# Optimization experiments

Measured on AMD Instinct MI355X. Metric: run time of the kernel, lower is better.

The kernel has to match this reference:

```python
import jax, jax.numpy as jnp
import numpy as np
from jax import lax

LEAK = 0.2
EPS = 1e-5
T = 20  # sequence_length


def _lrelu(x):
    return jnp.where(x >= 0, x, LEAK * x)


def _deconv(x, w, stride=2, k=4, p=1):
    # PyTorch ConvTranspose2d(weight [in,out,kH,kW], stride=2, pad=1) equivalent:
    # flip kernel spatially, swap in/out channels, use lhs_dilation.
    wt = jnp.flip(w, (2, 3)).transpose(1, 0, 2, 3)  # OIHW
    pad = k - 1 - p
    return lax.conv_general_dilated(
        x, wt, window_strides=(1, 1), padding=[(pad, pad), (pad, pad)],
        lhs_dilation=(stride, stride),
        dimension_numbers=('NCHW', 'OIHW', 'NCHW'))


def _bn(x, g, b):
    # BatchNorm2d, training mode (batch statistics, biased variance)
    m = x.mean((0, 2, 3), keepdims=True)
    v = x.var((0, 2, 3), keepdims=True)
    return (x - m) * lax.rsqrt(v + EPS) * g[None, :, None, None] + b[None, :, None, None]


def setup_inputs() -> dict:
    B, CD, MD, H, FF = 64, 128, 128, 256, 512
    ks = jax.random.split(jax.random.key(0), 32)
    rn = lambda k, sh, s=0.02: (s * jax.random.normal(k, sh)).astype(jnp.float32)
    return {
        'z_content': jax.random.normal(ks[0], (B, CD), jnp.float32),
        'z_motion': jax.random.normal(ks[1], (B, MD), jnp.float32),
        'W_h': rn(ks[2], (H, CD + MD)), 'b_h': jnp.zeros((H,), jnp.float32),
        'W_c': rn(ks[3], (H, CD + MD)), 'b_c': jnp.zeros((H,), jnp.float32),
        'W_ih': rn(ks[4], (4 * H, H)), 'W_hh': rn(ks[5], (4 * H, H)),
        'b_ih': jnp.zeros((4 * H,), jnp.float32), 'b_hh': jnp.zeros((4 * H,), jnp.float32),
        'W_f': rn(ks[6], (FF, H)), 'b_f': jnp.zeros((FF,), jnp.float32),
        'init_in': rn(ks[7], (1, H), 0.1),
        'fc_W': rn(ks[8], (256 * 4 * 4, FF + CD)), 'fc_b': jnp.zeros((256 * 16,), jnp.float32),
        'w0': rn(ks[9], (256, 128, 4, 4)), 'g0': jnp.ones((128,), jnp.float32), 'be0': jnp.zeros((128,), jnp.float32),
        'w1': rn(ks[10], (128, 64, 4, 4)), 'g1': jnp.ones((64,), jnp.float32), 'be1': jnp.zeros((64,), jnp.float32),
        'w2': rn(ks[11], (64, 32, 4, 4)), 'g2': jnp.ones((32,), jnp.float32), 'be2': jnp.zeros((32,), jnp.float32),
        'wf': rn(ks[12], (32, 1, 4, 4)), 'bf': jnp.zeros((1,), jnp.float32),
    }


def reference(z_content, z_motion, W_h, b_h, W_c, b_c, W_ih, W_hh, b_ih, b_hh,
              W_f, b_f, init_in, fc_W, fc_b, w0, g0, be0, w1, g1, be1,
              w2, g2, be2, wf, bf):
    B = z_content.shape[0]
    z = jnp.concatenate([z_content, z_motion], axis=-1)
    h0 = z @ W_h.T + b_h  # [B,H]
    c0 = z @ W_c.T + b_c
    x0 = jnp.broadcast_to(init_in, (B, init_in.shape[1]))
    bias = b_ih + b_hh

    def step(carry, _):
        x, h, c = carry
        gates = x @ W_ih.T + h @ W_hh.T + bias  # [B,4H], torch gate order i,f,g,o
        i, f, g, o = jnp.split(gates, 4, axis=-1)
        c_new = jax.nn.sigmoid(f) * c + jax.nn.sigmoid(i) * jnp.tanh(g)
        h_new = jax.nn.sigmoid(o) * jnp.tanh(c_new)
        return (h_new, h_new, c_new), h_new

    _, outs = lax.scan(step, (x0, h0, c0), None, length=T)  # [T,B,H]
    outs = outs.transpose(1, 0, 2)  # [B,T,H]

    ff = _lrelu(outs @ W_f.T + b_f)  # [B,T,FF]
    zc = jnp.broadcast_to(z_content[:, None, :], (B, T, z_content.shape[1]))
    feat = jnp.concatenate([ff, zc], axis=-1).reshape(B * T, -1)  # [B*T, FF+CD]

    h = _lrelu(feat @ fc_W.T + fc_b).reshape(B * T, 256, 4, 4)
    h = _lrelu(_bn(_deconv(h, w0), g0, be0))   # [B*T,128,8,8]
    h = _lrelu(_bn(_deconv(h, w1), g1, be1))   # [B*T,64,16,16]
    h = _lrelu(_bn(_deconv(h, w2), g2, be2))   # [B*T,32,32,32]
    out = jax.nn.sigmoid(_deconv(h, wf) + bf[None, :, None, None])  # [B*T,1,64,64]
    return out.reshape(B, T, *out.shape[1:])
```

## Files before the change

kernel.cpp:

```cpp
#include <hip/hip_runtime.h>
#include <hip/hip_bf16.h>
#include <math.h>

typedef __hip_bfloat16 bf16;
typedef __attribute__((ext_vector_type(8))) short bf16x8;
typedef __attribute__((ext_vector_type(4))) float f32x4;
typedef __attribute__((ext_vector_type(2))) float f32x2;

#define LRELU(v) ((v) > 0.f ? (v) : 0.2f*(v))

__device__ __forceinline__ float sig_f(float x){ return 1.f/(1.f + __expf(-x)); }
__device__ __forceinline__ float tanh_f(float x){
  float ax = fabsf(x);
  float e = __expf(-2.f*ax);
  float t = (1.f - e)/(1.f + e);
  return x >= 0.f ? t : -t;
}
__device__ __forceinline__ ushort bfbits(float v){
  bf16 b = __float2bfloat16(v);
  return *(ushort*)&b;
}
__device__ __forceinline__ uint bfpack(float a, float b){
  return (uint)bfbits(a) | ((uint)bfbits(b) << 16);
}
__device__ __forceinline__ float bflo(uint u){ return __uint_as_float(u << 16); }
__device__ __forceinline__ float bfhi(uint u){ return __uint_as_float(u & 0xffff0000u); }

template<int CI, int CO>
__device__ __forceinline__ void wprep_body(const float* __restrict__ w,
                                           ushort* __restrict__ wpn, int e){
  constexpr int K = 4*CI, KF = K/32, MMW2 = CO/16;
  if (e >= 16*CI*CO) return;
  int j  = e & 7;
  int lk = (e >> 3) & 3;
  int lm = (e >> 5) & 15;
  int r3 = e >> 9;
  int kf = r3 % KF; int r4 = r3 / KF;
  int m  = r4 % MMW2; int p = r4 / MMW2;
  int k  = kf*32 + lk*8 + j;
  int t  = k / CI, ci = k % CI;
  int co = m*16 + lm;
  int py = p >> 1, px = p & 1, dy = t >> 1, dx = t & 1;
  int ky = (py ? 0 : 1) + 2*dy;
  int kx = (px ? 0 : 1) + 2*dx;
  wpn[e] = bfbits(w[((ci*CO + co)*4 + ky)*4 + kx]);
}

__global__ __launch_bounds__(256) void k_prep(
    const float* __restrict__ W_h, const float* __restrict__ W_c,
    float* __restrict__ WhT, float* __restrict__ WcT,
    const float* __restrict__ fc_W, ushort* __restrict__ wpfc,
    const float* __restrict__ W_f, ushort* __restrict__ wpff,
    const float* __restrict__ Wih, const float* __restrict__ Whh,
    uint4* __restrict__ Whq8, uint4* __restrict__ Wsq8, float* __restrict__ stats,
    const float* __restrict__ b_ih, const float* __restrict__ b_hh,
    const float* __restrict__ init_in,
    float4* __restrict__ xg4, float4* __restrict__ bias4,
    const float* __restrict__ w0, ushort* __restrict__ wp0,
    const float* __restrict__ w1, ushort* __restrict__ wp1,
    const float* __restrict__ w2, ushort* __restrict__ wp2,
    const float* __restrict__ wf, ushort* __restrict__ wfb)
{
  __shared__ float t[32][33];
  __shared__ float4 red[4];
  const int b = blockIdx.x, tid = threadIdx.x;

  if (b < 128) {
    const float* src = (b < 64) ? W_h : W_c;
    float* dst = (b < 64) ? WhT : WcT;
    int bb = b & 63;
    int c0 = (bb & 7)*32, r0 = (bb >> 3)*32;
    int tx = tid & 31, ty = tid >> 5;
    #pragma unroll
    for (int i = 0; i < 4; ++i)
      t[ty+8*i][tx] = src[(size_t)(r0+ty+8*i)*256 + c0+tx];
    __syncthreads();
    #pragma unroll
    for (int i = 0; i < 4; ++i)
      dst[(size_t)(c0+ty+8*i)*256 + r0+tx] = t[tx][ty+8*i];
    return;
  }
  if (b < 10368) {
    int i = (b - 128)*256 + tid;
    if (i < 2621440) wpfc[i] = bfbits(fc_W[i]);
    return;
  }
  if (b < 10880) {
    int i = (b - 10368)*256 + tid;
    if (i < 131072) wpff[i] = bfbits(W_f[i]);
    return;
  }
  if (b < 10944) {
    int k4 = b - 10880, j = tid;
    if (k4 < 2) { int i = k4*256 + j; if (i < 448) stats[i] = 0.f; }
    uint h4[4], s4[4];
    #pragma unroll
    for (int d = 0; d < 4; ++d) {
      int k = 4*k4 + d;
      float hi = Whh[j*256+k],       hf = Whh[(256+j)*256+k];
      float hg = Whh[(512+j)*256+k], ho = Whh[(768+j)*256+k];
      float ii = Wih[j*256+k],       iff = Wih[(256+j)*256+k];
      float ig = Wih[(512+j)*256+k], io = Wih[(768+j)*256+k];
      int lo = __builtin_amdgcn_cvt_pk_fp8_f32(hi, hf, 0, false);
      h4[d] = (uint)__builtin_amdgcn_cvt_pk_fp8_f32(hg, ho, lo, true);
      lo = __builtin_amdgcn_cvt_pk_fp8_f32(hi+ii, hf+iff, 0, false);
      s4[d] = (uint)__builtin_amdgcn_cvt_pk_fp8_f32(hg+ig, ho+io, lo, true);
    }
    Whq8[k4*256+j] = make_uint4(h4[0], h4[1], h4[2], h4[3]);
    Wsq8[k4*256+j] = make_uint4(s4[0], s4[1], s4[2], s4[3]);
    return;
  }
  if (b < 11200) {
    int bb = b - 10944, tt = tid;
    float v = init_in[tt];
    float p0 = v * Wih[bb*256 + tt];
    float p1 = v * Wih[(256+bb)*256 + tt];
    float p2 = v * Wih[(512+bb)*256 + tt];
    float p3 = v * Wih[(768+bb)*256 + tt];
    #pragma unroll
    for (int o = 32; o; o >>= 1) {
      p0 += __shfl_xor(p0, o); p1 += __shfl_xor(p1, o);
      p2 += __shfl_xor(p2, o); p3 += __shfl_xor(p3, o);
    }
    int lane = tt & 63, wid = tt >> 6;
    if (lane == 0) red[wid] = make_float4(p0,p1,p2,p3);
    __syncthreads();
    if (tt == 0) {
      float4 bi = make_float4(b_ih[bb]+b_hh[bb], b_ih[256+bb]+b_hh[256+bb],
                              b_ih[512+bb]+b_hh[512+bb], b_ih[768+bb]+b_hh[768+bb]);
      bias4[bb] = bi;
      float4 a = bi;
      #pragma unroll
      for (int w = 0; w < 4; ++w) { a.x += red[w].x; a.y += red[w].y; a.z += red[w].z; a.w += red[w].w; }
      xg4[bb] = a;
    }
    return;
  }
  if (b < 13248) { wprep_body<256,128>(w0, wp0, (b - 11200)*256 + tid); return; }
  if (b < 13760) { wprep_body<128,64>(w1, wp1, (b - 13248)*256 + tid); return; }
  if (b < 13888) { wprep_body<64,32>(w2, wp2, (b - 13760)*256 + tid); return; }
  {
    int e = (b - 13888)*256 + tid;
    if (e < 512) {
      int tt = e >> 5, ci = e & 31;
      wfb[tt*32 + ci] = bfbits(wf[ci*16 + tt]);
    }
  }
}

__global__ __launch_bounds__(256) void k_h0c0(const float* __restrict__ zc, const float* __restrict__ zm,
                      const float* __restrict__ WhT, const float* __restrict__ WcT,
                      const float* __restrict__ b_h, const float* __restrict__ b_c,
                      float* __restrict__ h, float* __restrict__ c){
  __shared__ float zs[256];
  int b = blockIdx.x, j = threadIdx.x;
  zs[j] = (j < 128) ? zc[b*128 + j] : zm[b*128 + (j-128)];
  __syncthreads();
  float ah = b_h[j], ac = b_c[j];
  #pragma unroll 4
  for (int k = 0; k < 256; ++k) {
    float zv = zs[k];
    ah = fmaf(zv, WhT[k*256 + j], ah);
    ac = fmaf(zv, WcT[k*256 + j], ac);
  }
  h[b*256+j] = ah; c[b*256+j] = ac;
}

__global__ __launch_bounds__(1024) void k_lstm_all(
    const uint4* __restrict__ Whq8, const uint4* __restrict__ Wsq8,
    const float4* __restrict__ xg4, const float4* __restrict__ bias4,
    const float* __restrict__ h0, const float* __restrict__ c0,
    ushort* __restrict__ outsb){
  __shared__ float hs[256];
  __shared__ float4 part[3][256];
  const int b = blockIdx.x, tid = threadIdx.x;
  const int j = tid & 255, kq = tid >> 8;
  float cj = 0.f;
  if (kq == 0) { hs[j] = h0[b*256 + j]; cj = c0[b*256 + j]; }
  __syncthreads();
  for (int t = 0; t < 20; ++t) {
    const uint4* __restrict__ Wp = ((t == 0) ? Whq8 : Wsq8) + (size_t)(kq*16)*256 + j;
    float4 a = make_float4(0.f, 0.f, 0.f, 0.f);
    #pragma unroll 8
    for (int kk = 0; kk < 16; ++kk) {
      uint4 wv = Wp[(size_t)kk*256];
      const float* __restrict__ hb = &hs[kq*64 + 4*kk];
      {
        f32x2 pif = __builtin_amdgcn_cvt_pk_f32_fp8((int)wv.x, false);
        f32x2 pgo = __builtin_amdgcn_cvt_pk_f32_fp8((int)wv.x, true);
        float hv = hb[0];
        a.x = fmaf(hv, pif[0], a.x); a.y = fmaf(hv, pif[1], a.y);
        a.z = fmaf(hv, pgo[0], a.z); a.w = fmaf(hv, pgo[1], a.w);
      }
      {
        f32x2 pif = __builtin_amdgcn_cvt_pk_f32_fp8((int)wv.y, false);
        f32x2 pgo = __builtin_amdgcn_cvt_pk_f32_fp8((int)wv.y, true);
        float hv = hb[1];
        a.x = fmaf(hv, pif[0], a.x); a.y = fmaf(hv, pif[1], a.y);
        a.z = fmaf(hv, pgo[0], a.z); a.w = fmaf(hv, pgo[1], a.w);
      }
      {
        f32x2 pif = __builtin_amdgcn_cvt_pk_f32_fp8((int)wv.z, false);
        f32x2 pgo = __builtin_amdgcn_cvt_pk_f32_fp8((int)wv.z, true);
        float hv = hb[2];
        a.x = fmaf(hv, pif[0], a.x); a.y = fmaf(hv, pif[1], a.y);
        a.z = fmaf(hv, pgo[0], a.z); a.w = fmaf(hv, pgo[1], a.w);
      }
      {
        f32x2 pif = __builtin_amdgcn_cvt_pk_f32_fp8((int)wv.w, false);
        f32x2 pgo = __builtin_amdgcn_cvt_pk_f32_fp8((int)wv.w, true);
        float hv = hb[3];
        a.x = fmaf(hv, pif[0], a.x); a.y = fmaf(hv, pif[1], a.y);
        a.z = fmaf(hv, pgo[0], a.z); a.w = fmaf(hv, pgo[1], a.w);
      }
    }
    if (kq) part[kq-1][j] = a;
    __syncthreads();
    if (kq == 0) {
      float4 p1 = part[0][j], p2 = part[1][j], p3 = part[2][j];
      float4 bb = (t == 0) ? xg4[j] : bias4[j];
      a.x += p1.x + p2.x + p3.x + bb.x;
      a.y += p1.y + p2.y + p3.y + bb.y;
      a.z += p1.z + p2.z + p3.z + bb.z;
      a.w += p1.w + p2.w + p3.w + bb.w;
      float ig = sig_f(a.x), fg = sig_f(a.y), gg = tanh_f(a.z), og = sig_f(a.w);
      cj = fmaf(fg, cj, ig*gg);
      float hj = og * tanh_f(cj);
      outsb[(b*20 + t)*256 + j] = bfbits(hj);
      hs[j] = hj;
    }
    __syncthreads();
  }
}

__global__ __launch_bounds__(256) void k_ff_m(
    const ushort* __restrict__ A, const ushort* __restrict__ W,
    const float* __restrict__ bias, const float* __restrict__ zc,
    ushort* __restrict__ C)
{
  constexpr int K = 256, BK = 64, NK = K/BK, BM = 128, BN = 64;
  constexpr int RS = 72;
  constexpr int NCF = BN/16;
  constexpr int AC = 4, WC = 2;

  __shared__ __align__(16) ushort Al[2][BM*RS];
  __shared__ __align__(16) ushort Wl[2][BN*RS];

  const int tid = threadIdx.x;
  const int col0 = blockIdx.x * BN, row0 = blockIdx.y * BM;
  const int w = tid >> 6, l = tid & 63, lm = l & 15, lk = l >> 4;

  f32x4 acc[NCF][2];
  #pragma unroll
  for (int m = 0; m < NCF; ++m)
    #pragma unroll
    for (int s = 0; s < 2; ++s)
      acc[m][s] = (f32x4){0.f,0.f,0.f,0.f};

  uint4 ar[AC], wr[WC];

  #define LOADG(kt) { \
    _Pragma("unroll") \
    for (int i = 0; i < AC; ++i) { \
      int chunk = tid + i*256; \
      int rl = chunk >> 3, kc = chunk & 7; \
      ar[i] = *(const uint4*)&A[(size_t)(row0+rl)*K + (kt)*BK + kc*8]; \
    } \
    _Pragma("unroll") \
    for (int i = 0; i < WC; ++i) { \
      int chunk = tid + i*256; \
      int co = chunk >> 3, kc = chunk & 7; \
      wr[i] = *(const uint4*)&W[(size_t)(col0+co)*K + (kt)*BK + kc*8]; \
    } }

  #define STOREL(buf) { \
    _Pragma("unroll") \
    for (int i = 0; i < AC; ++i) { \
      int chunk = tid + i*256; \
      int rl = chunk >> 3, kc = chunk & 7; \
      *(uint4*)&Al[buf][rl*RS + kc*8] = ar[i]; \
    } \
    _Pragma("unroll") \
    for (int i = 0; i < WC; ++i) { \
      int chunk = tid + i*256; \
      int co = chunk >> 3, kc = chunk & 7; \
      *(uint4*)&Wl[buf][co*RS + kc*8] = wr[i]; \
    } }

  LOADG(0);
  STOREL(0);
  int cur = 0;
  for (int kt = 0; kt < NK; ++kt) {
    if (kt + 1 < NK) LOADG(kt + 1);
    __syncthreads();
    #pragma unroll
    for (int kf = 0; kf < 2; ++kf) {
      bf16x8 bfr[2];
      #pragma unroll
      for (int s = 0; s < 2; ++s)
        bfr[s] = *(bf16x8*)&Al[cur][(w*32 + s*16 + lm)*RS + kf*32 + lk*8];
      #pragma unroll
      for (int m = 0; m < NCF; ++m) {
        bf16x8 afr = *(bf16x8*)&Wl[cur][(m*16 + lm)*RS + kf*32 + lk*8];
        acc[m][0] = __builtin_amdgcn_mfma_f32_16x16x32_bf16(afr, bfr[0], acc[m][0], 0, 0, 0);
        acc[m][1] = __builtin_amdgcn_mfma_f32_16x16x32_bf16(afr, bfr[1], acc[m][1], 0, 0, 0);
      }
    }
    if (kt + 1 < NK) STOREL(cur ^ 1);
    cur ^= 1;
  }

  #pragma unroll
  for (int m = 0; m < NCF; ++m) {
    #pragma unroll
    for (int s = 0; s < 2; ++s) {
      int row = row0 + w*32 + s*16 + lm;
      f32x4 v = acc[m][s];
      int u0 = col0 + m*16 + lk*4;
      union { ushort u[4]; uint2 q; } pk;
      #pragma unroll
      for (int j = 0; j < 4; ++j)
        pk.u[j] = bfbits(LRELU(v[j] + bias[u0+j]));
      *(uint2*)&C[(size_t)row*640 + u0] = pk.q;
    }
  }
  {
    int base = ((int)blockIdx.y*8 + (int)blockIdx.x)*2048 + tid;
    #pragma unroll
    for (int i = 0; i < 8; ++i) {
      int e = base + i*256;
      int r = e >> 7, c2 = e & 127;
      C[r*640 + 512 + c2] = bfbits(zc[(r/20)*128 + c2]);
    }
  }
  #undef LOADG
  #undef STOREL
}

__global__ __launch_bounds__(256) void k_gemm_fc_m(
    const ushort* __restrict__ A, const ushort* __restrict__ W,
    const float* __restrict__ bias, ushort* __restrict__ C)
{
  constexpr int K = 640, BK = 64, NK = K/BK, BM = 128, BN = 64;
  constexpr int RS = 72;
  constexpr int NCF = BN/16;
  constexpr int AC = 4, WC = 2;

  __shared__ __align__(16) ushort Al[2][BM*RS];
  __shared__ __align__(16) ushort Wl[2][BN*RS];

  const int tid = threadIdx.x;
  const int col0 = blockIdx.x * BN, row0 = blockIdx.y * BM;
  const int w = tid >> 6, l = tid & 63, lm = l & 15, lk = l >> 4;

  f32x4 acc[NCF][2];
  #pragma unroll
  for (int m = 0; m < NCF; ++m)
    #pragma unroll
    for (int s = 0; s < 2; ++s)
      acc[m][s] = (f32x4){0.f,0.f,0.f,0.f};

  uint4 ar[AC], wr[WC];

  #define LOADG(kt) { \
    _Pragma("unroll") \
    for (int i = 0; i < AC; ++i) { \
      int chunk = tid + i*256; \
      int rl = chunk >> 3, kc = chunk & 7; \
      ar[i] = *(const uint4*)&A[(size_t)(row0+rl)*K + (kt)*BK + kc*8]; \
    } \
    _Pragma("unroll") \
    for (int i = 0; i < WC; ++i) { \
      int chunk = tid + i*256; \
      int co = chunk >> 3, kc = chunk & 7; \
      wr[i] = *(const uint4*)&W[(size_t)(col0+co)*K + (kt)*BK + kc*8]; \
    } }

  #define STOREL(buf) { \
    _Pragma("unroll") \
    for (int i = 0; i < AC; ++i) { \
      int chunk = tid + i*256; \
      int rl = chunk >> 3, kc = chunk & 7; \
      *(uint4*)&Al[buf][rl*RS + kc*8] = ar[i]; \
    } \
    _Pragma("unroll") \
    for (int i = 0; i < WC; ++i) { \
      int chunk = tid + i*256; \
      int co = chunk >> 3, kc = chunk & 7; \
      *(uint4*)&Wl[buf][co*RS + kc*8] = wr[i]; \
    } }

  LOADG(0);
  STOREL(0);
  int cur = 0;
  for (int kt = 0; kt < NK; ++kt) {
    if (kt + 1 < NK) LOADG(kt + 1);
    __syncthreads();
    #pragma unroll
    for (int kf = 0; kf < 2; ++kf) {
      bf16x8 bfr[2];
      #pragma unroll
      for (int s = 0; s < 2; ++s)
        bfr[s] = *(bf16x8*)&Al[cur][(w*32 + s*16 + lm)*RS + kf*32 + lk*8];
      #pragma unroll
      for (int m = 0; m < NCF; ++m) {
        bf16x8 afr = *(bf16x8*)&Wl[cur][(m*16 + lm)*RS + kf*32 + lk*8];
        acc[m][0] = __builtin_amdgcn_mfma_f32_16x16x32_bf16(afr, bfr[0], acc[m][0], 0, 0, 0);
        acc[m][1] = __builtin_amdgcn_mfma_f32_16x16x32_bf16(afr, bfr[1], acc[m][1], 0, 0, 0);
      }
    }
    if (kt + 1 < NK) STOREL(cur ^ 1);
    cur ^= 1;
  }

  #pragma unroll
  for (int m = 0; m < NCF; ++m) {
    #pragma unroll
    for (int s = 0; s < 2; ++s) {
      int row = row0 + w*32 + s*16 + lm;
      f32x4 v = acc[m][s];
      #pragma unroll
      for (int j = 0; j < 4; ++j) {
        int u = col0 + m*16 + lk*4 + j;
        float val = LRELU(v[j] + bias[u]);
        C[((size_t)row << 12) + ((size_t)(u & 15) << 8) + (u >> 4)] = bfbits(val);
      }
    }
  }
  #undef LOADG
  #undef STOREL
}

template<int CI, int CO, int HI>
__global__ __attribute__((amdgpu_flat_work_group_size(256, 256), amdgpu_waves_per_eu(2, 4)))
void k_dcv(
    const ushort* __restrict__ in, const ushort* __restrict__ wp,
    ushort* __restrict__ out, float* __restrict__ gsum, float* __restrict__ gsq)
{
  constexpr int WI = HI, HO = 2*HI, WO = 2*WI;
  constexpr int K = 4*CI, KFT = K/32;
  constexpr int BSP = 128;
  constexpr int NCF = CO/32;
  constexpr int COH = CO/2;

  __shared__ float s_sum[COH], s_sq[COH];

  const int tid = threadIdx.x;
  const int sp0 = blockIdx.x * BSP;
  const int p  = blockIdx.y;
  const int coz = blockIdx.z;
  const int py = p >> 1, px = p & 1;
  const int w  = tid >> 6, l = tid & 63;
  const int lm = l & 15, lk = l >> 4;

  if (tid < COH) { s_sum[tid] = 0.f; s_sq[tid] = 0.f; }

  f32x4 acc[NCF][2];
  #pragma unroll
  for (int m = 0; m < NCF; ++m)
    #pragma unroll
    for (int s = 0; s < 2; ++s)
      acc[m][s] = (f32x4){0.f,0.f,0.f,0.f};

  int pn[2], poy[2], pox[2];
  #pragma unroll
  for (int s = 0; s < 2; ++s) {
    int sp = sp0 + w*32 + s*16 + lm;
    pn[s] = sp / (HI*WI);
    int rem = sp % (HI*WI);
    poy[s] = rem / WI; pox[s] = rem % WI;
  }

  const ushort* wpb = wp + (size_t)(p*(CO/16) + coz*NCF)*KFT*512;

  bf16x8 afrN[NCF];
  #pragma unroll
  for (int m = 0; m < NCF; ++m)
    afrN[m] = *(const bf16x8*)&wpb[((size_t)m*KFT)*512 + lm*32 + lk*8];

  for (int ktg = 0; ktg < KFT; ++ktg) {
    const int t = (ktg*32)/CI;
    const int ci0 = (ktg*32)%CI + lk*8;
    const int dy = t >> 1, dx = t & 1;
    bf16x8 afr[NCF];
    #pragma unroll
    for (int m = 0; m < NCF; ++m) afr[m] = afrN[m];
    if (ktg + 1 < KFT) {
      #pragma unroll
      for (int m = 0; m < NCF; ++m)
        afrN[m] = *(const bf16x8*)&wpb[((size_t)m*KFT + ktg + 1)*512 + lm*32 + lk*8];
    }
    bf16x8 bfr[2];
    #pragma unroll
    for (int s = 0; s < 2; ++s) {
      int iy = poy[s] + py - dy, ix = pox[s] + px - dx;
      bool valid = ((unsigned)iy < (unsigned)HI) && ((unsigned)ix < (unsigned)WI);
      if (valid)
        bfr[s] = *(const bf16x8*)&in[((((size_t)pn[s]*HI + iy)*WI + ix)*CI) + ci0];
      else
        bfr[s] = (bf16x8){0,0,0,0,0,0,0,0};
    }
    #pragma unroll
    for (int m = 0; m < NCF; ++m) {
      acc[m][0] = __builtin_amdgcn_mfma_f32_16x16x32_bf16(afr[m], bfr[0], acc[m][0], 0, 0, 0);
      acc[m][1] = __builtin_amdgcn_mfma_f32_16x16x32_bf16(afr[m], bfr[1], acc[m][1], 0, 0, 0);
    }
  }

  #pragma unroll
  for (int m = 0; m < NCF; ++m) {
    float s1[4] = {0,0,0,0}, s2[4] = {0,0,0,0};
    #pragma unroll
    for (int s = 0; s < 2; ++s) {
      f32x4 v = acc[m][s];
      #pragma unroll
      for (int j = 0; j < 4; ++j) { s1[j] += v[j]; s2[j] += v[j]*v[j]; }
    }
    #pragma unroll
    for (int j = 0; j < 4; ++j) {
      float a = s1[j], b = s2[j];
      #pragma unroll
      for (int o = 1; o < 16; o <<= 1) { a += __shfl_xor(a, o); b += __shfl_xor(b, o); }
      if (lm == 0) {
        atomicAdd(&s_sum[m*16 + lk*4 + j], a);
        atomicAdd(&s_sq [m*16 + lk*4 + j], b);
      }
    }
  }
  #pragma unroll
  for (int s = 0; s < 2; ++s) {
    int y = 2*poy[s] + py, x = 2*pox[s] + px;
    size_t ob = (((size_t)pn[s]*HO + y)*WO + x)*CO + coz*COH + lk*4;
    #pragma unroll
    for (int m = 0; m < NCF; ++m) {
      f32x4 v = acc[m][s];
      union { ushort u[4]; uint2 q; } pk;
      pk.u[0] = bfbits(v[0]); pk.u[1] = bfbits(v[1]);
      pk.u[2] = bfbits(v[2]); pk.u[3] = bfbits(v[3]);
      *(uint2*)&out[ob + m*16] = pk.q;
    }
  }
  __syncthreads();
  for (int cc = tid; cc < COH; cc += 256) {
    atomicAdd(&gsum[coz*COH + cc], s_sum[cc]);
    atomicAdd(&gsq[coz*COH + cc],  s_sq[cc]);
  }
}

template<int CI, int CO, int HI>
__global__ __attribute__((amdgpu_flat_work_group_size(512, 512), amdgpu_waves_per_eu(2, 4)))
void k_dcvim(
    const ushort* __restrict__ in, const ushort* __restrict__ wp,
    const float* __restrict__ gsumP, const float* __restrict__ gsqP,
    const float* __restrict__ gP, const float* __restrict__ beP, float invNP,
    ushort* __restrict__ out, float* __restrict__ gsum, float* __restrict__ gsq)
{
  constexpr int WI = HI, HO = 2*HI, WO = 2*WI;
  constexpr int K = 4*CI;
  constexpr int KF = K/32;
  constexpr int PAD = HI + 2;
  constexpr int CICH = CI/8;
  constexpr int MMW2 = CO/16;
  constexpr int SFTH = HI*WI/32;

  __shared__ __align__(16) ushort Ain[PAD*PAD*CI];
  __shared__ float s_sum[CO], s_sq[CO];
  __shared__ float s_scale[CI], s_shift[CI];

  const int tid = threadIdx.x;
  const int n = blockIdx.x;
  const int w = tid >> 6, l = tid & 63, lm = l & 15, lk = l >> 4;
  const int p = w >> 1, py = p >> 1, px = p & 1, ph = w & 1;

  if (tid < CO) { s_sum[tid] = 0.f; s_sq[tid] = 0.f; }
  if (tid >= 512-CI) {
    int c = tid - (512-CI);
    float m = gsumP[c]*invNP;
    float v = gsqP[c]*invNP - m*m;
    float sc = gP[c]*rsqrtf(v + 1e-5f);
    s_scale[c] = sc;
    s_shift[c] = beP[c] - m*sc;
  }
  __syncthreads();

  const ushort* inb = in + (size_t)n * HI * WI * CI;
  constexpr int NPCH = PAD*PAD*CICH;
  for (int e = tid; e < NPCH; e += 512) {
    int ci8 = e % CICH; int sp = e / CICH;
    int c = sp % PAD, r = sp / PAD;
    int chS = ci8 ^ (c & 7);
    if (r >= 1 && r <= HI && c >= 1 && c <= WI) {
      uint4 u = *(const uint4*)&inb[(((size_t)(r-1)*WI + (c-1))*CI) + ci8*8];
      int ci0 = ci8*8;
      float4 sc0 = *(const float4*)&s_scale[ci0];
      float4 sc1 = *(const float4*)&s_scale[ci0+4];
      float4 sh0 = *(const float4*)&s_shift[ci0];
      float4 sh1 = *(const float4*)&s_shift[ci0+4];
      float v0 = LRELU(fmaf(bflo(u.x), sc0.x, sh0.x));
      float v1 = LRELU(fmaf(bfhi(u.x), sc0.y, sh0.y));
      float v2 = LRELU(fmaf(bflo(u.y), sc0.z, sh0.z));
      float v3 = LRELU(fmaf(bfhi(u.y), sc0.w, sh0.w));
      float v4 = LRELU(fmaf(bflo(u.z), sc1.x, sh1.x));
      float v5 = LRELU(fmaf(bfhi(u.z), sc1.y, sh1.y));
      float v6 = LRELU(fmaf(bflo(u.w), sc1.z, sh1.z));
      float v7 = LRELU(fmaf(bfhi(u.w), sc1.w, sh1.w));
      uint4 o;
      o.x = (uint)bfpack(v0, v1);
      o.y = (uint)bfpack(v2, v3);
      o.z = (uint)bfpack(v4, v5);
      o.w = (uint)bfpack(v6, v7);
      ((uint4*)Ain)[(r*PAD + c)*CICH + chS] = o;
    } else {
      ((uint4*)Ain)[(r*PAD + c)*CICH + chS] = make_uint4(0,0,0,0);
    }
  }
  __syncthreads();

  f32x4 acc[MMW2][SFTH];
  #pragma unroll
  for (int m = 0; m < MMW2; ++m)
    #pragma unroll
    for (int sf = 0; sf < SFTH; ++sf)
      acc[m][sf] = (f32x4){0.f,0.f,0.f,0.f};

  const ushort* wpb = wp + (size_t)(p*MMW2)*KF*512;
  bf16x8 afrN[MMW2];
  #pragma unroll
  for (int m = 0; m < MMW2; ++m)
    afrN[m] = *(const bf16x8*)&wpb[((size_t)m*KF)*512 + lm*32 + lk*8];
  #pragma unroll
  for (int kf = 0; kf < KF; ++kf) {
    const int t = (kf*32)/CI, cib = (kf*32)%CI;
    const int dy = t >> 1, dx = t & 1;
    bf16x8 afr[MMW2];
    #pragma unroll
    for (int m = 0; m < MMW2; ++m) afr[m] = afrN[m];
    if (kf + 1 < KF) {
      #pragma unroll
      for (int m = 0; m < MMW2; ++m)
        afrN[m] = *(const bf16x8*)&wpb[((size_t)m*KF + (kf+1))*512 + lm*32 + lk*8];
    }
    const int ch = (cib >> 3) + lk;
    #pragma unroll
    for (int sf = 0; sf < SFTH; ++sf) {
      int s = (ph*SFTH + sf)*16 + lm;
      int y = s / WI, x = s % WI;
      int r = y + py - dy + 1, c = x + px - dx + 1;
      bf16x8 bfr = *(const bf16x8*)&Ain[((r*PAD + c)*CICH + (ch ^ (c & 7)))*8];
      #pragma unroll
      for (int m = 0; m < MMW2; ++m)
        acc[m][sf] = __builtin_amdgcn_mfma_f32_16x16x32_bf16(afr[m], bfr, acc[m][sf], 0, 0, 0);
    }
  }

  float s1[MMW2][4], s2[MMW2][4];
  #pragma unroll
  for (int m = 0; m < MMW2; ++m)
    #pragma unroll
    for (int j = 0; j < 4; ++j) { s1[m][j] = 0.f; s2[m][j] = 0.f; }

  #pragma unroll
  for (int sf = 0; sf < SFTH; ++sf) {
    int s = (ph*SFTH + sf)*16 + lm;
    int y = 2*(s / WI) + py, x = 2*(s % WI) + px;
    size_t ob = (((size_t)n*HO + y)*WO + x)*CO + lk*4;
    #pragma unroll
    for (int m = 0; m < MMW2; ++m) {
      f32x4 v = acc[m][sf];
      union { ushort u[4]; uint2 q; } pk;
      #pragma unroll
      for (int j = 0; j < 4; ++j) {
        pk.u[j] = bfbits(v[j]);
        s1[m][j] += v[j];
        s2[m][j] += v[j]*v[j];
      }
      *(uint2*)&out[ob + m*16] = pk.q;
    }
  }

  #pragma unroll
  for (int m = 0; m < MMW2; ++m) {
    #pragma unroll
    for (int j = 0; j < 4; ++j) {
      float a = s1[m][j], b = s2[m][j];
      #pragma unroll
      for (int o = 1; o < 16; o <<= 1) { a += __shfl_xor(a, o); b += __shfl_xor(b, o); }
      if (lm == 0) {
        atomicAdd(&s_sum[m*16 + lk*4 + j], a);
        atomicAdd(&s_sq [m*16 + lk*4 + j], b);
      }
    }
  }

  __syncthreads();
  for (int cc = tid; cc < CO; cc += 512) {
    atomicAdd(&gsum[cc], s_sum[cc]);
    atomicAdd(&gsq[cc],  s_sq[cc]);
  }
}

__global__ __launch_bounds__(256) void k_final(
    const ushort* __restrict__ in, const ushort* __restrict__ wfb,
    const float* __restrict__ gsumP, const float* __restrict__ gsqP,
    const float* __restrict__ gP, const float* __restrict__ beP, float invNP,
    const float* __restrict__ bfb, float* __restrict__ outp)
{
  constexpr int CI=32, HI=32, WI=32, HO=64, WO=64, SPLIT=4, HOq=HO/SPLIT;
  constexpr int RMAX = 10;
  constexpr int DP = 20;
  __shared__ float Dl[RMAX*32*DP];
  __shared__ float s_scale[CI], s_shift[CI];

  const int tid = threadIdx.x, bid = blockIdx.x;
  const int n = bid % 1280, q = bid / 1280;
  const int y0 = q * HOq;
  const int rows_lo = max(0, y0/2 - 1);
  const int rows_hi = min(HI-1, (y0 + HOq)/2);
  const int nrows = rows_hi - rows_lo + 1;

  if (tid < CI) {
    float m = gsumP[tid]*invNP;
    float v = gsqP[tid]*invNP - m*m;
    float sc = gP[tid]*rsqrtf(v + 1e-5f);
    s_scale[tid] = sc;
    s_shift[tid] = beP[tid] - m*sc;
  }
  __syncthreads();

  const int w = tid >> 6, l = tid & 63, lm = l & 15, lk = l >> 4;
  const bf16x8 afr = *(const bf16x8*)&wfb[lm*32 + lk*8];
  const float4 sc0 = *(const float4*)&s_scale[lk*8];
  const float4 sc1 = *(const float4*)&s_scale[lk*8+4];
  const float4 sh0 = *(const float4*)&s_shift[lk*8];
  const float4 sh1 = *(const float4*)&s_shift[lk*8+4];

  const ushort* inb = in + (size_t)n * HI * WI * CI;
  const int ngrp = nrows * 2;
  for (int g = w; g < ngrp; g += 4) {
    int px = g*16 + lm;
    int rl = px >> 5, ix = px & 31;
    uint4 u = *(const uint4*)&inb[(((size_t)(rows_lo+rl)*WI + ix)*CI) + lk*8];
    float v0 = LRELU(fmaf(bflo(u.x), sc0.x, sh0.x));
    float v1 = LRELU(fmaf(bfhi(u.x), sc0.y, sh0.y));
    float v2 = LRELU(fmaf(bflo(u.y), sc0.z, sh0.z));
    float v3 = LRELU(fmaf(bfhi(u.y), sc0.w, sh0.w));
    float v4 = LRELU(fmaf(bflo(u.z), sc1.x, sh1.x));
    float v5 = LRELU(fmaf(bfhi(u.z), sc1.y, sh1.y));
    float v6 = LRELU(fmaf(bflo(u.w), sc1.z, sh1.z));
    float v7 = LRELU(fmaf(bfhi(u.w), sc1.w, sh1.w));
    union { uint uu[4]; bf16x8 v; } pk;
    pk.uu[0] = bfpack(v0, v1);
    pk.uu[1] = bfpack(v2, v3);
    pk.uu[2] = bfpack(v4, v5);
    pk.uu[3] = bfpack(v6, v7);
    f32x4 d = __builtin_amdgcn_mfma_f32_16x16x32_bf16(afr, pk.v, (f32x4){0.f,0.f,0.f,0.f}, 0, 0, 0);
    *(f32x4*)&Dl[px*DP + lk*4] = d;
  }
  __syncthreads();

  const float b0 = bfb[0];
  #pragma unroll
  for (int i = 0; i < (HOq*WO)/256; ++i) {
    int e = tid + i*256;
    int oy = e >> 6, x = e & 63;
    int y = y0 + oy;
    int kya = (y + 1) & 1, iya = (y + 1) >> 1;
    int kxa = (x + 1) & 1, ixa = (x + 1) >> 1;
    float acc = b0;
    #pragma unroll
    for (int dy = 0; dy < 2; ++dy) {
      int iy = iya - dy, ky = kya + 2*dy;
      if (iy < 0 || iy >= HI) continue;
      #pragma unroll
      for (int dx = 0; dx < 2; ++dx) {
        int ix = ixa - dx, kx = kxa + 2*dx;
        if (ix < 0 || ix >= WI) continue;
        acc += Dl[((iy - rows_lo)*WI + ix)*DP + (ky*4 + kx)];
      }
    }
    outp[(size_t)n*HO*WO + y*WO + x] = 1.f/(1.f + __expf(-acc));
  }
}

extern "C" void kernel_launch(void* const* d_in, const int* in_sizes, int n_in,
                              void* d_out, int out_size, void* d_ws, size_t ws_size,
                              hipStream_t stream) {
  const float* z_content = (const float*)d_in[0];
  const float* z_motion  = (const float*)d_in[1];
  const float* W_h  = (const float*)d_in[2];
  const float* b_h  = (const float*)d_in[3];
  const float* W_c  = (const float*)d_in[4];
  const float* b_c  = (const float*)d_in[5];
  const float* W_ih = (const float*)d_in[6];
  const float* W_hh = (const float*)d_in[7];
  const float* b_ih = (const float*)d_in[8];
  const float* b_hh = (const float*)d_in[9];
  const float* W_f  = (const float*)d_in[10];
  const float* b_f  = (const float*)d_in[11];
  const float* init_in = (const float*)d_in[12];
  const float* fc_W = (const float*)d_in[13];
  const float* fc_b = (const float*)d_in[14];
  const float* w0 = (const float*)d_in[15];
  const float* g0 = (const float*)d_in[16];
  const float* be0 = (const float*)d_in[17];
  const float* w1 = (const float*)d_in[18];
  const float* g1 = (const float*)d_in[19];
  const float* be1 = (const float*)d_in[20];
  const float* w2 = (const float*)d_in[21];
  const float* g2 = (const float*)d_in[22];
  const float* be2 = (const float*)d_in[23];
  const float* wf = (const float*)d_in[24];
  const float* bf_ = (const float*)d_in[25];

  const size_t P_BYTES = 10631168;
  const size_t X_OFF   = P_BYTES;
  const size_t X_BYTES = 83886080;
  const size_t Y_OFF   = X_OFF + X_BYTES;
  const size_t NEED    = Y_OFF + 41943040;
  if (ws_size < NEED) return;

  float* ws = (float*)d_ws;
  char*  wsb = (char*)d_ws;
  float* sum0 = ws + 0;        float* sq0 = ws + 128;
  float* sum1 = ws + 256;      float* sq1 = ws + 320;
  float* sum2 = ws + 384;      float* sq2 = ws + 416;
  float4* xg4   = (float4*)(ws + 1024);
  float4* bias4 = (float4*)(ws + 2048);
  float* h    = ws + 3072;
  float* c    = ws + 19456;
  ushort* outsb = (ushort*)(ws + 35840);
  float* WhT  = ws + 199680;
  float* WcT  = ws + 265216;
  uint4* Whq8 = (uint4*)(ws + 330752);
  uint4* Wsq8 = (uint4*)(ws + 592896);
  ushort* wp0 = (ushort*)(ws + 855040);
  ushort* wp1 = (ushort*)(ws + 1117184);
  ushort* wp2 = (ushort*)(ws + 1182720);
  ushort* wfb = (ushort*)(ws + 1199104);
  ushort* wpff = (ushort*)(ws + 1199616);
  ushort* featb = (ushort*)(ws + 1265152);

  ushort* wpfc = (ushort*)(wsb + X_OFF);
  ushort* out0 = (ushort*)(wsb + X_OFF);
  ushort* out2 = (ushort*)(wsb + X_OFF);
  ushort* h1   = (ushort*)(wsb + Y_OFF);
  ushort* out1 = (ushort*)(wsb + Y_OFF);

  k_prep<<<13890, 256, 0, stream>>>(
      W_h, W_c, WhT, WcT, fc_W, wpfc, W_f, wpff,
      W_ih, W_hh, Whq8, Wsq8, ws, b_ih, b_hh, init_in, xg4, bias4,
      w0, wp0, w1, wp1, w2, wp2, wf, wfb);
  k_h0c0<<<64, 256, 0, stream>>>(z_content, z_motion, WhT, WcT, b_h, b_c, h, c);

  k_lstm_all<<<64, 1024, 0, stream>>>(Whq8, Wsq8, xg4, bias4, h, c, outsb);

  k_ff_m<<<dim3(8, 10), 256, 0, stream>>>(outsb, wpff, b_f, z_content, featb);
  k_gemm_fc_m<<<dim3(64, 10), 256, 0, stream>>>(featb, wpfc, fc_b, h1);

  k_dcv<256,128,4><<<dim3(160,4,2), 256, 0, stream>>>(h1, wp0, out0, sum0, sq0);
  k_dcvim<128,64,8><<<1280, 512, 0, stream>>>(out0, wp1, sum0, sq0, g0, be0, 1.f/81920.f, out1, sum1, sq1);
  k_dcvim<64,32,16><<<1280, 512, 0, stream>>>(out1, wp2, sum1, sq1, g1, be1, 1.f/327680.f, out2, sum2, sq2);
  k_final<<<5120, 256, 0, stream>>>(out2, wfb, sum2, sq2, g2, be2, 1.f/1310720.f, bf_, (float*)d_out);
}
```

Baseline: 414.2 us.

## Stage first deconv input images in swizzled LDS, one image per wave

The first transposed-conv layer (4x4 -> 8x8) now loads four whole input images per block into shared memory with an XOR swizzle. Each wave then computes one image's 16 output positions for its parity, reading B fragments from LDS instead of doing bounds-checked global loads. The K loop is fully unrolled and the grid doubles to 320 blocks along x, since each block now covers 64 positions instead of 128. In exchange, each wave issues half as many MFMAs per A-fragment load, which lowers weight reuse, and the kernel needs 32KB of LDS per block.

```diff
diff --git a/kernel.cpp b/kernel.cpp
--- a/kernel.cpp
+++ b/kernel.cpp
@@ -433,44 +433,43 @@
 
 template<int CI, int CO, int HI>
 __global__ __attribute__((amdgpu_flat_work_group_size(256, 256), amdgpu_waves_per_eu(2, 4)))
-void k_dcv(
+void k_dcv0(
     const ushort* __restrict__ in, const ushort* __restrict__ wp,
     ushort* __restrict__ out, float* __restrict__ gsum, float* __restrict__ gsq)
 {
   constexpr int WI = HI, HO = 2*HI, WO = 2*WI;
-  constexpr int K = 4*CI, KFT = K/32;
-  constexpr int BSP = 128;
+  constexpr int KFT = 4*CI/32;
   constexpr int NCF = CO/32;
   constexpr int COH = CO/2;
-
+  constexpr int CICH = CI/8;
+
+  __shared__ __align__(16) ushort Ain[4*16*CI];
   __shared__ float s_sum[COH], s_sq[COH];
 
   const int tid = threadIdx.x;
-  const int sp0 = blockIdx.x * BSP;
-  const int p  = blockIdx.y;
+  const int n0 = blockIdx.x * 4;
+  const int p = blockIdx.y, py = p >> 1, pxp = p & 1;
   const int coz = blockIdx.z;
-  const int py = p >> 1, px = p & 1;
-  const int w  = tid >> 6, l = tid & 63;
-  const int lm = l & 15, lk = l >> 4;
+  const int w = tid >> 6, l = tid & 63, lm = l & 15, lk = l >> 4;
 
   if (tid < COH) { s_sum[tid] = 0.f; s_sq[tid] = 0.f; }
 
-  f32x4 acc[NCF][2];
-  #pragma unroll
-  for (int m = 0; m < NCF; ++m)
-    #pragma unroll
-    for (int s = 0; s < 2; ++s)
-      acc[m][s] = (f32x4){0.f,0.f,0.f,0.f};
-
-  int pn[2], poy[2], pox[2];
-  #pragma unroll
-  for (int s = 0; s < 2; ++s) {
-    int sp = sp0 + w*32 + s*16 + lm;
-    pn[s] = sp / (HI*WI);
-    int rem = sp % (HI*WI);
-    poy[s] = rem / WI; pox[s] = rem % WI;
-  }
-
+  const ushort* inb = in + (size_t)n0 * 16 * CI;
+  #pragma unroll
+  for (int i = 0; i < 8; ++i) {
+    int e = tid + i*256;
+    int ci8 = e & 31; int sp = e >> 5;
+    uint4 u = *(const uint4*)&inb[(size_t)sp*CI + ci8*8];
+    int px = sp & 15;
+    ((uint4*)Ain)[sp*CICH + (ci8 ^ (px & 7))] = u;
+  }
+  __syncthreads();
+
+  f32x4 acc[NCF];
+  #pragma unroll
+  for (int m = 0; m < NCF; ++m) acc[m] = (f32x4){0.f,0.f,0.f,0.f};
+
+  const int oy = lm >> 2, ox = lm & 3;
   const ushort* wpb = wp + (size_t)(p*(CO/16) + coz*NCF)*KFT*512;
 
   bf16x8 afrN[NCF];
@@ -478,47 +477,35 @@
   for (int m = 0; m < NCF; ++m)
     afrN[m] = *(const bf16x8*)&wpb[((size_t)m*KFT)*512 + lm*32 + lk*8];
 
-  for (int ktg = 0; ktg < KFT; ++ktg) {
-    const int t = (ktg*32)/CI;
-    const int ci0 = (ktg*32)%CI + lk*8;
+  #pragma unroll
+  for (int kf = 0; kf < KFT; ++kf) {
+    const int t = kf >> 3;
     const int dy = t >> 1, dx = t & 1;
+    const int ch = ((kf & 7) << 2) + lk;
     bf16x8 afr[NCF];
     #pragma unroll
     for (int m = 0; m < NCF; ++m) afr[m] = afrN[m];
-    if (ktg + 1 < KFT) {
+    if (kf + 1 < KFT) {
       #pragma unroll
       for (int m = 0; m < NCF; ++m)
-        afrN[m] = *(const bf16x8*)&wpb[((size_t)m*KFT + ktg + 1)*512 + lm*32 + lk*8];
-    }
-    bf16x8 bfr[2];
-    #pragma unroll
-    for (int s = 0; s < 2; ++s) {
-      int iy = poy[s] + py - dy, ix = pox[s] + px - dx;
-      bool valid = ((unsigned)iy < (unsigned)HI) && ((unsigned)ix < (unsigned)WI);
-      if (valid)
-        bfr[s] = *(const bf16x8*)&in[((((size_t)pn[s]*HI + iy)*WI + ix)*CI) + ci0];
-      else
-        bfr[s] = (bf16x8){0,0,0,0,0,0,0,0};
-    }
-    #pragma unroll
-    for (int m = 0; m < NCF; ++m) {
-      acc[m][0] = __builtin_amdgcn_mfma_f32_16x16x32_bf16(afr[m], bfr[0], acc[m][0], 0, 0, 0);
-      acc[m][1] = __builtin_amdgcn_mfma_f32_16x16x32_bf16(afr[m], bfr[1], acc[m][1], 0, 0, 0);
-    }
+        afrN[m] = *(const bf16x8*)&wpb[((size_t)m*KFT + kf + 1)*512 + lm*32 + lk*8];
+    }
+    int iy = oy + py - dy, ix = ox + pxp - dx;
+    bool valid = ((unsigned)iy < 4u) && ((unsigned)ix < 4u);
+    int pix = iy*4 + ix;
+    bf16x8 bfr = (bf16x8){0,0,0,0,0,0,0,0};
+    if (valid)
+      bfr = *(const bf16x8*)&Ain[((w*16 + pix)*CICH + (ch ^ (pix & 7)))*8];
+    #pragma unroll
+    for (int m = 0; m < NCF; ++m)
+      acc[m] = __builtin_amdgcn_mfma_f32_16x16x32_bf16(afr[m], bfr, acc[m], 0, 0, 0);
   }
 
   #pragma unroll
   for (int m = 0; m < NCF; ++m) {
-    float s1[4] = {0,0,0,0}, s2[4] = {0,0,0,0};
-    #pragma unroll
-    for (int s = 0; s < 2; ++s) {
-      f32x4 v = acc[m][s];
-      #pragma unroll
-      for (int j = 0; j < 4; ++j) { s1[j] += v[j]; s2[j] += v[j]*v[j]; }
-    }
     #pragma unroll
     for (int j = 0; j < 4; ++j) {
-      float a = s1[j], b = s2[j];
+      float a = acc[m][j], b = acc[m][j]*acc[m][j];
       #pragma unroll
       for (int o = 1; o < 16; o <<= 1) { a += __shfl_xor(a, o); b += __shfl_xor(b, o); }
       if (lm == 0) {
@@ -527,13 +514,13 @@
       }
     }
   }
-  #pragma unroll
-  for (int s = 0; s < 2; ++s) {
-    int y = 2*poy[s] + py, x = 2*pox[s] + px;
-    size_t ob = (((size_t)pn[s]*HO + y)*WO + x)*CO + coz*COH + lk*4;
+  {
+    int n = n0 + w;
+    int y = 2*oy + py, x = 2*ox + pxp;
+    size_t ob = (((size_t)n*HO + y)*WO + x)*CO + coz*COH + lk*4;
     #pragma unroll
     for (int m = 0; m < NCF; ++m) {
-      f32x4 v = acc[m][s];
+      f32x4 v = acc[m];
       union { ushort u[4]; uint2 q; } pk;
       pk.u[0] = bfbits(v[0]); pk.u[1] = bfbits(v[1]);
       pk.u[2] = bfbits(v[2]); pk.u[3] = bfbits(v[3]);
@@ -857,7 +844,7 @@
   k_ff_m<<<dim3(8, 10), 256, 0, stream>>>(outsb, wpff, b_f, z_content, featb);
   k_gemm_fc_m<<<dim3(64, 10), 256, 0, stream>>>(featb, wpfc, fc_b, h1);
 
-  k_dcv<256,128,4><<<dim3(160,4,2), 256, 0, stream>>>(h1, wp0, out0, sum0, sq0);
+  k_dcv0<256,128,4><<<dim3(320,4,2), 256, 0, stream>>>(h1, wp0, out0, sum0, sq0);
   k_dcvim<128,64,8><<<1280, 512, 0, stream>>>(out0, wp1, sum0, sq0, g0, be0, 1.f/81920.f, out1, sum1, sq1);
   k_dcvim<64,32,16><<<1280, 512, 0, stream>>>(out1, wp2, sum1, sq1, g1, be1, 1.f/327680.f, out2, sum2, sq2);
   k_final<<<5120, 256, 0, stream>>>(out2, wfb, sum2, sq2, g2, be2, 1.f/1310720.f, bf_, (float*)d_out);
```

Result: no change. 416.3 us (+0.5%).
